# Kernel tuning notes

Hardware: AMD Instinct MI355X
Metric: run time of the kernel (lower is better)

The kernel has to match this reference:

```python
import jax, jax.numpy as jnp
import numpy as np

HIDDEN = 1280
NUM_HEADS = 16
NUM_KV_HEADS = 4
HEAD_DIM = 80
Q_SIZE = NUM_HEADS * HEAD_DIM          # 1280
KV_SIZE = NUM_KV_HEADS * HEAD_DIM      # 320
QKV_OUT = Q_SIZE + 2 * KV_SIZE         # 1920
R_SOFTPLUS_0 = 1.442695041


def setup_inputs() -> dict:
    key = jax.random.key(0)
    ks = jax.random.split(key, 6)
    B, S = 4, 2048
    return {
        "hidden_states": jax.random.normal(ks[0], (B, S, HIDDEN), dtype=jnp.float32),
        "scaling": jax.random.normal(ks[1], (HEAD_DIM,), dtype=jnp.float32),
        "qkv_w": jax.random.normal(ks[2], (QKV_OUT, HIDDEN), dtype=jnp.float32) * (1.0 / np.sqrt(HIDDEN)),
        "qkv_b": jax.random.normal(ks[3], (QKV_OUT,), dtype=jnp.float32) * 0.01,
        "o_w": jax.random.normal(ks[4], (HIDDEN, Q_SIZE), dtype=jnp.float32) * (1.0 / np.sqrt(Q_SIZE)),
        "o_b": jax.random.normal(ks[5], (HIDDEN,), dtype=jnp.float32) * 0.01,
    }


def reference(hidden_states, scaling, qkv_w, qkv_b, o_w, o_b):
    B, S, _ = hidden_states.shape
    qkv = hidden_states @ qkv_w.T + qkv_b                      # [B,S,1920]
    xq = qkv[..., :Q_SIZE].reshape(B, S, NUM_HEADS, HEAD_DIM)
    xk = qkv[..., Q_SIZE:Q_SIZE + KV_SIZE].reshape(B, S, NUM_KV_HEADS, HEAD_DIM)
    xv = qkv[..., Q_SIZE + KV_SIZE:].reshape(B, S, NUM_KV_HEADS, HEAD_DIM)
    # learned per-head-dim scaling: (r_softplus_0/sqrt(d)) * softplus(scaling)
    scale = (R_SOFTPLUS_0 / np.sqrt(HEAD_DIM)) * jax.nn.softplus(scaling)
    xq = xq * scale[None, None, None, :]
    # GQA: expand kv heads to match query heads (repeat_interleave on head dim)
    nq_per_kv = NUM_HEADS // NUM_KV_HEADS
    k = jnp.repeat(xk, nq_per_kv, axis=2)                      # [B,S,H,d]
    v = jnp.repeat(xv, nq_per_kv, axis=2)
    scores = jnp.einsum("bqhd,bkhd->bhqk", xq, k)              # [B,H,S,S]
    probs = jax.nn.softmax(scores.astype(jnp.float32), axis=-1).astype(xq.dtype)
    out = jnp.einsum("bhqk,bkhd->bqhd", probs, v)              # [B,S,H,d]
    out = out.reshape(B, S, Q_SIZE)
    return out @ o_w.T + o_b
```

## Files before the change

### kernel.cpp

```cpp
#include <hip/hip_runtime.h>

#define HIDDEN 1280
#define QOUT   1920
#define QSIZE  1280
#define KVSIZE 320
#define NHEAD  16
#define NKV    4
#define DH     80
#define SEQ    2048
#define BATCH  4
#define MTOT   (BATCH * SEQ)
#define NT64   (SEQ / 64)
#define KTILE_ELEMS 6144
#define VTILE_ELEMS 5120

typedef __attribute__((ext_vector_type(8))) short bf16x8;
typedef __attribute__((ext_vector_type(4))) short bf16x4;
typedef __attribute__((ext_vector_type(4))) float f32x4;

__device__ __forceinline__ unsigned short f2bf(float x) {
  union { float f; unsigned u; } v; v.f = x;
  unsigned r = v.u + 0x7fffu + ((v.u >> 16) & 1u);
  return (unsigned short)(r >> 16);
}

__device__ __forceinline__ unsigned packbf(float a, float b) {
  union { float f; unsigned u; } ua, ub;
  ua.f = a; ub.f = b;
  return __builtin_amdgcn_perm(ub.u + 0x8000u, ua.u + 0x8000u, 0x07060302u);
}

__device__ __forceinline__ unsigned packbf_t(float a, float b) {
  union { float f; unsigned u; } ua, ub;
  ua.f = a; ub.f = b;
  return __builtin_amdgcn_perm(ub.u, ua.u, 0x07060302u);
}

__device__ __forceinline__ float exp2x(float x) {
#if __has_builtin(__builtin_amdgcn_exp2f)
  return __builtin_amdgcn_exp2f(x);
#else
  return exp2f(x);
#endif
}

__device__ __forceinline__ void async_copy16(const void* g, void* lds) {
  __builtin_amdgcn_global_load_lds(
      (const __attribute__((address_space(1))) unsigned int*)g,
      (__attribute__((address_space(3))) unsigned int*)lds, 16, 0, 0);
}

#define HSB   (MTOT * HIDDEN / 4 / 256)
#define QWB   (QOUT * HIDDEN / 4 / 256)
#define OWB   (HIDDEN * QSIZE / 4 / 256)
__global__ __launch_bounds__(256) void prep_k(const float* __restrict__ hs,
                                              const float* __restrict__ qkv_w,
                                              const float* __restrict__ o_w,
                                              const float* __restrict__ scaling,
                                              unsigned short* __restrict__ hs_bf,
                                              unsigned short* __restrict__ qkvw_bf,
                                              unsigned short* __restrict__ ow_bf,
                                              float* __restrict__ cs) {
  const int bid = blockIdx.x, tid = threadIdx.x;
  const float* src; unsigned short* dst; int i;
  if (bid < HSB)            { src = hs;    dst = hs_bf;   i = bid * 256 + tid; }
  else if (bid < HSB + QWB) { src = qkv_w; dst = qkvw_bf; i = (bid - HSB) * 256 + tid; }
  else if (bid < HSB + QWB + OWB) { src = o_w; dst = ow_bf; i = (bid - HSB - QWB) * 256 + tid; }
  else {
    int n = (bid - HSB - QWB - OWB) * 256 + tid;
    if (n < QOUT) {
      float v = 1.0f;
      if (n < QSIZE) {
        float x = scaling[n % DH];
        float sp = (x > 20.f) ? x : log1pf(__expf(x));
        v = 1.442695041f * 1.442695041f * 0.11180339887f * sp;
      }
      cs[n] = v;
    }
    return;
  }
  float4 v = ((const float4*)src)[i];
  ushort4 o;
  o.x = f2bf(v.x); o.y = f2bf(v.y); o.z = f2bf(v.z); o.w = f2bf(v.w);
  ((ushort4*)dst)[i] = o;
}

template <bool OUT_BF16, bool USE_SCALE>
__global__ __launch_bounds__(512) void gemm_bt(const unsigned short* __restrict__ A,
                                               const unsigned short* __restrict__ Bt,
                                               const float* __restrict__ bias,
                                               const float* __restrict__ colscale,
                                               void* __restrict__ Cout,
                                               int M, int N, int K) {
  __shared__ unsigned short As[256 * 64];
  __shared__ unsigned short Bs[128 * 64];
  const int tid  = threadIdx.x;
  const int wave = tid >> 6, lane = tid & 63;
  const int r = lane & 15, quad = lane >> 4;
  const int xm = r & 7;
  const int m0 = blockIdx.y * 256, n0 = blockIdx.x * 128;
  const int rm = (wave >> 1) * 64, cn = (wave & 1) * 64;

  f32x4 acc[4][4];
#pragma unroll
  for (int i = 0; i < 4; ++i)
#pragma unroll
    for (int j = 0; j < 4; ++j) acc[i][j] = f32x4{0.f, 0.f, 0.f, 0.f};

  for (int k0 = 0; k0 < K; k0 += 64) {
    __syncthreads();
#pragma unroll
    for (int j = 0; j < 4; ++j) {
      const int c = tid + j * 512;
      const int row = c >> 3, sp = c & 7;
      const int sd = (sp ^ (row & 7)) * 8;
      async_copy16(A + (size_t)(m0 + row) * K + k0 + sd, &As[c * 8]);
    }
#pragma unroll
    for (int j = 0; j < 2; ++j) {
      const int c = tid + j * 512;
      const int row = c >> 3, sp = c & 7;
      const int sd = (sp ^ (row & 7)) * 8;
      async_copy16(Bt + (size_t)(n0 + row) * K + k0 + sd, &Bs[c * 8]);
    }
    __syncthreads();
#pragma unroll
    for (int kk = 0; kk < 2; ++kk) {
      bf16x8 af[4], bfr[4];
#pragma unroll
      for (int mi = 0; mi < 4; ++mi)
        af[mi] = *(const bf16x8*)&As[(rm + mi * 16 + r) * 64 + ((kk * 4 + quad) ^ xm) * 8];
#pragma unroll
      for (int ni = 0; ni < 4; ++ni)
        bfr[ni] = *(const bf16x8*)&Bs[(cn + ni * 16 + r) * 64 + ((kk * 4 + quad) ^ xm) * 8];
#pragma unroll
      for (int mi = 0; mi < 4; ++mi)
#pragma unroll
        for (int ni = 0; ni < 4; ++ni)
          acc[mi][ni] = __builtin_amdgcn_mfma_f32_16x16x32_bf16(af[mi], bfr[ni], acc[mi][ni], 0, 0, 0);
    }
  }

#pragma unroll
  for (int ni = 0; ni < 4; ++ni) {
    const int n = n0 + cn + ni * 16 + r;
    const float bn = bias[n];
    const float sc = USE_SCALE ? colscale[n] : 1.0f;
#pragma unroll
    for (int mi = 0; mi < 4; ++mi) {
#pragma unroll
      for (int reg = 0; reg < 4; ++reg) {
        const int m = m0 + rm + mi * 16 + quad * 4 + reg;
        const float v = (acc[mi][ni][reg] + bn) * sc;
        if (OUT_BF16)
          ((unsigned short*)Cout)[(size_t)m * N + n] = f2bf(v);
        else
          ((float*)Cout)[(size_t)m * N + n] = v;
      }
    }
  }
}

__global__ __launch_bounds__(256) void kvpack(const unsigned short* __restrict__ qkv,
                                              unsigned short* __restrict__ Kp,
                                              unsigned short* __restrict__ Vp) {
  const int st = blockIdx.x, kvh = blockIdx.y, b = blockIdx.z;
  const int tid = threadIdx.x;
  unsigned short* kout = Kp + (size_t)((b * NKV + kvh) * NT64 + st) * KTILE_ELEMS;
#pragma unroll
  for (int j = 0; j < 3; ++j) {
    int c = tid + j * 256;
    int row = c / 12, cir = c - row * 12;
    int kk = cir >> 2, sp = cir & 3;
    int sd = sp ^ ((row >> 1) & 3);
    int d0 = kk * 32 + sd * 8;
    int skey = (row >> 5) * 32 + ((row >> 2) & 3) * 8 + ((row >> 4) & 1) * 4 + (row & 3);
    uint4 v = {0, 0, 0, 0};
    if (d0 < DH)
      v = *(const uint4*)&qkv[(size_t)(b * SEQ + st * 64 + skey) * QOUT +
                              QSIZE + kvh * DH + d0];
    *(uint4*)&kout[row * 96 + kk * 32 + sp * 8] = v;
  }
  __shared__ unsigned short tile[64][88];
  for (int c = tid; c < 640; c += 256) {
    int row = c / 10, seg = c % 10;
    uint4 v = *(const uint4*)&qkv[(size_t)(b * SEQ + st * 64 + row) * QOUT +
                                  QSIZE + KVSIZE + kvh * DH + seg * 8];
    *(uint4*)&tile[row][seg * 8] = v;
  }
  __syncthreads();
  unsigned short* vout = Vp + (size_t)((b * NKV + kvh) * NT64 + st) * VTILE_ELEMS;
  for (int c = tid; c < 5120; c += 256) {
    int d = c >> 6, key = c & 63;
    vout[d * 64 + (key ^ ((d & 7) << 3))] = tile[key][d];
  }
}

__global__ __launch_bounds__(256, 2) void attn(const unsigned short* __restrict__ qkv,
                                               const unsigned short* __restrict__ Kp,
                                               const unsigned short* __restrict__ Vp,
                                               unsigned short* __restrict__ att) {
  const int qt = blockIdx.x, h = blockIdx.y, b = blockIdx.z;
  const int kvh = h >> 2;
  const int tid = threadIdx.x;
  const int wave = tid >> 6, lane = tid & 63;
  const int r = lane & 15, quad = lane >> 4;
  const int sq8 = (quad ^ ((r >> 1) & 3)) * 8;

  __shared__ unsigned short Ks[64 * 96];
  __shared__ unsigned short Vs[96 * 64];

  {
    const uint4 ones = {0x3F803F80u, 0x3F803F80u, 0x3F803F80u, 0x3F803F80u};
    for (int c = tid; c < 128; c += 256)
      *(uint4*)&Vs[80 * 64 + c * 8] = ones;
  }

  const int qbase = qt * 256 + wave * 64;
  bf16x8 qb[4][3];
#pragma unroll
  for (int t = 0; t < 4; ++t)
#pragma unroll
    for (int kk = 0; kk < 3; ++kk)
      qb[t][kk] = *(const bf16x8*)&qkv[(size_t)(b * SEQ + qbase + t * 16 + r) * QOUT +
                                       h * DH + kk * 32 + quad * 8];

  f32x4 o_acc[6][4];
#pragma unroll
  for (int i = 0; i < 6; ++i)
#pragma unroll
    for (int t = 0; t < 4; ++t) o_acc[i][t] = f32x4{0.f, 0.f, 0.f, 0.f};

  const unsigned short* kp = Kp + (size_t)((b * NKV + kvh) * NT64) * KTILE_ELEMS;
  const unsigned short* vp = Vp + (size_t)((b * NKV + kvh) * NT64) * VTILE_ELEMS;

  for (int kt = 0; kt < NT64; ++kt) {
    __syncthreads();
#pragma unroll
    for (int j = 0; j < 3; ++j)
      async_copy16(kp + (size_t)kt * KTILE_ELEMS + (tid + j * 256) * 8,
                   &Ks[(tid + j * 256) * 8]);
#pragma unroll
    for (int j = 0; j < 3; ++j) {
      int c = tid + j * 256;
      if (c < 640)
        async_copy16(vp + (size_t)kt * VTILE_ELEMS + c * 8, &Vs[c * 8]);
    }
    __syncthreads();

#pragma unroll
    for (int ntp = 0; ntp < 2; ++ntp) {
      uint4 pw[4];
      {
        bf16x8 ka[3];
#pragma unroll
        for (int kk = 0; kk < 3; ++kk)
          ka[kk] = *(const bf16x8*)&Ks[(ntp * 32 + r) * 96 + kk * 32 + sq8];
#pragma unroll
        for (int t = 0; t < 4; ++t) {
          f32x4 s = f32x4{0.f, 0.f, 0.f, 0.f};
#pragma unroll
          for (int kk = 0; kk < 3; ++kk)
            s = __builtin_amdgcn_mfma_f32_16x16x32_bf16(ka[kk], qb[t][kk], s, 0, 0, 0);
          pw[t].x = packbf_t(exp2x(s[0]), exp2x(s[1]));
          pw[t].y = packbf_t(exp2x(s[2]), exp2x(s[3]));
        }
      }
      {
        bf16x8 ka[3];
#pragma unroll
        for (int kk = 0; kk < 3; ++kk)
          ka[kk] = *(const bf16x8*)&Ks[(ntp * 32 + 16 + r) * 96 + kk * 32 + sq8];
#pragma unroll
        for (int t = 0; t < 4; ++t) {
          f32x4 s = f32x4{0.f, 0.f, 0.f, 0.f};
#pragma unroll
          for (int kk = 0; kk < 3; ++kk)
            s = __builtin_amdgcn_mfma_f32_16x16x32_bf16(ka[kk], qb[t][kk], s, 0, 0, 0);
          pw[t].z = packbf_t(exp2x(s[0]), exp2x(s[1]));
          pw[t].w = packbf_t(exp2x(s[2]), exp2x(s[3]));
        }
      }

#pragma unroll
      for (int nt2 = 0; nt2 < 6; ++nt2) {
        bf16x8 va = *(const bf16x8*)&Vs[(nt2 * 16 + r) * 64 +
                                        (((ntp * 4 + quad) ^ (r & 7)) << 3)];
#pragma unroll
        for (int t = 0; t < 4; ++t) {
          union { uint4 u; bf16x8 v; } pv; pv.u = pw[t];
          o_acc[nt2][t] = __builtin_amdgcn_mfma_f32_16x16x32_bf16(va, pv.v, o_acc[nt2][t], 0, 0, 0);
        }
      }
    }
  }

#pragma unroll
  for (int t = 0; t < 4; ++t) {
    const float il = 1.0f / o_acc[5][t][0];
    const size_t q = (size_t)(b * SEQ + qbase + t * 16 + r);
#pragma unroll
    for (int nt2 = 0; nt2 < 5; ++nt2) {
      uint2 w;
      w.x = packbf(o_acc[nt2][t][0] * il, o_acc[nt2][t][1] * il);
      w.y = packbf(o_acc[nt2][t][2] * il, o_acc[nt2][t][3] * il);
      *(uint2*)&att[q * QSIZE + h * DH + nt2 * 16 + quad * 4] = w;
    }
  }
}

extern "C" void kernel_launch(void* const* d_in, const int* in_sizes, int n_in,
                              void* d_out, int out_size, void* d_ws, size_t ws_size,
                              hipStream_t stream) {
  const float* hs      = (const float*)d_in[0];
  const float* scaling = (const float*)d_in[1];
  const float* qkv_w   = (const float*)d_in[2];
  const float* qkv_b   = (const float*)d_in[3];
  const float* o_w     = (const float*)d_in[4];
  const float* o_b     = (const float*)d_in[5];

  char* p = (char*)d_ws;
  unsigned short* hs_bf   = (unsigned short*)p; p += (size_t)MTOT * HIDDEN * 2;
  unsigned short* qkvw_bf = (unsigned short*)p; p += (size_t)QOUT * HIDDEN * 2;
  unsigned short* ow_bf   = (unsigned short*)p; p += (size_t)HIDDEN * QSIZE * 2;
  float* cscale           = (float*)p;          p += (size_t)QOUT * 4;
  unsigned short* qkv     = (unsigned short*)p; p += (size_t)MTOT * QOUT * 2;
  unsigned short* Kp      = (unsigned short*)p; p += (size_t)BATCH * NKV * NT64 * KTILE_ELEMS * 2;
  unsigned short* Vp      = (unsigned short*)p; p += (size_t)BATCH * NKV * NT64 * VTILE_ELEMS * 2;
  unsigned short* att     = hs_bf;

  prep_k<<<HSB + QWB + OWB + 8, 256, 0, stream>>>(hs, qkv_w, o_w, scaling,
                                                  hs_bf, qkvw_bf, ow_bf, cscale);

  dim3 g1(QOUT / 128, MTOT / 256);
  gemm_bt<true, true><<<g1, 512, 0, stream>>>(hs_bf, qkvw_bf, qkv_b, cscale, qkv,
                                              MTOT, QOUT, HIDDEN);
  dim3 gp(NT64, NKV, BATCH);
  kvpack<<<gp, 256, 0, stream>>>(qkv, Kp, Vp);
  dim3 g3(SEQ / 256, NHEAD, BATCH);
  attn<<<g3, 256, 0, stream>>>(qkv, Kp, Vp, att);
  dim3 g4(QSIZE / 128, MTOT / 256);
  gemm_bt<false, false><<<g4, 512, 0, stream>>>(att, ow_bf, o_b, nullptr, d_out,
                                                MTOT, QSIZE, HIDDEN);
}
```

Measured before the change: 283.6 us.

## Double-buffer K/V tiles in attention and split queries across eight waves

The attention kernel now keeps two LDS buffers for K and V and starts the async copy of the next key tile before computing on the current one. This overlaps global-to-LDS transfer with MFMA work and needs only one barrier per iteration. The block grows to 512 threads, each wave handling 32 queries instead of 64. That halves the per-wave accumulator and Q registers so more waves can hide latency, at the cost of less reuse of each K/V LDS fragment and twice the LDS footprint.

```diff
diff --git a/kernel.cpp b/kernel.cpp
--- a/kernel.cpp
+++ b/kernel.cpp
@@ -196,7 +196,7 @@
   }
 }
 
-__global__ __launch_bounds__(256, 2) void attn(const unsigned short* __restrict__ qkv,
+__global__ __launch_bounds__(512, 4) void attn(const unsigned short* __restrict__ qkv,
                                                const unsigned short* __restrict__ Kp,
                                                const unsigned short* __restrict__ Vp,
                                                unsigned short* __restrict__ att) {
@@ -207,57 +207,59 @@
   const int r = lane & 15, quad = lane >> 4;
   const int sq8 = (quad ^ ((r >> 1) & 3)) * 8;
 
-  __shared__ unsigned short Ks[64 * 96];
-  __shared__ unsigned short Vs[96 * 64];
+  __shared__ unsigned short Ks[2][64 * 96];
+  __shared__ unsigned short Vs[2][96 * 64];
 
   {
     const uint4 ones = {0x3F803F80u, 0x3F803F80u, 0x3F803F80u, 0x3F803F80u};
-    for (int c = tid; c < 128; c += 256)
-      *(uint4*)&Vs[80 * 64 + c * 8] = ones;
-  }
-
-  const int qbase = qt * 256 + wave * 64;
-  bf16x8 qb[4][3];
-#pragma unroll
-  for (int t = 0; t < 4; ++t)
+    for (int c = tid; c < 256; c += 512)
+      *(uint4*)&Vs[c >> 7][80 * 64 + (c & 127) * 8] = ones;
+  }
+
+  const int qbase = qt * 256 + wave * 32;
+  bf16x8 qb[2][3];
+#pragma unroll
+  for (int t = 0; t < 2; ++t)
 #pragma unroll
     for (int kk = 0; kk < 3; ++kk)
       qb[t][kk] = *(const bf16x8*)&qkv[(size_t)(b * SEQ + qbase + t * 16 + r) * QOUT +
                                        h * DH + kk * 32 + quad * 8];
 
-  f32x4 o_acc[6][4];
+  f32x4 o_acc[6][2];
 #pragma unroll
   for (int i = 0; i < 6; ++i)
 #pragma unroll
-    for (int t = 0; t < 4; ++t) o_acc[i][t] = f32x4{0.f, 0.f, 0.f, 0.f};
+    for (int t = 0; t < 2; ++t) o_acc[i][t] = f32x4{0.f, 0.f, 0.f, 0.f};
 
   const unsigned short* kp = Kp + (size_t)((b * NKV + kvh) * NT64) * KTILE_ELEMS;
   const unsigned short* vp = Vp + (size_t)((b * NKV + kvh) * NT64) * VTILE_ELEMS;
 
+#define STAGE(bufi, kt_) do {                                                   \
+    const unsigned short* kpt = kp + (size_t)(kt_) * KTILE_ELEMS;               \
+    async_copy16(kpt + tid * 8, &Ks[bufi][tid * 8]);                            \
+    if (tid < 256) async_copy16(kpt + (tid + 512) * 8, &Ks[bufi][(tid + 512) * 8]); \
+    const unsigned short* vpt = vp + (size_t)(kt_) * VTILE_ELEMS;               \
+    async_copy16(vpt + tid * 8, &Vs[bufi][tid * 8]);                            \
+    if (tid < 128) async_copy16(vpt + (tid + 512) * 8, &Vs[bufi][(tid + 512) * 8]); \
+  } while (0)
+
+  STAGE(0, 0);
+  __syncthreads();
+
   for (int kt = 0; kt < NT64; ++kt) {
-    __syncthreads();
-#pragma unroll
-    for (int j = 0; j < 3; ++j)
-      async_copy16(kp + (size_t)kt * KTILE_ELEMS + (tid + j * 256) * 8,
-                   &Ks[(tid + j * 256) * 8]);
-#pragma unroll
-    for (int j = 0; j < 3; ++j) {
-      int c = tid + j * 256;
-      if (c < 640)
-        async_copy16(vp + (size_t)kt * VTILE_ELEMS + c * 8, &Vs[c * 8]);
-    }
-    __syncthreads();
+    const int cur = kt & 1;
+    if (kt + 1 < NT64) STAGE(cur ^ 1, kt + 1);
 
 #pragma unroll
     for (int ntp = 0; ntp < 2; ++ntp) {
-      uint4 pw[4];
+      uint4 pw[2];
       {
         bf16x8 ka[3];
 #pragma unroll
         for (int kk = 0; kk < 3; ++kk)
-          ka[kk] = *(const bf16x8*)&Ks[(ntp * 32 + r) * 96 + kk * 32 + sq8];
-#pragma unroll
-        for (int t = 0; t < 4; ++t) {
+          ka[kk] = *(const bf16x8*)&Ks[cur][(ntp * 32 + r) * 96 + kk * 32 + sq8];
+#pragma unroll
+        for (int t = 0; t < 2; ++t) {
           f32x4 s = f32x4{0.f, 0.f, 0.f, 0.f};
 #pragma unroll
           for (int kk = 0; kk < 3; ++kk)
@@ -270,9 +272,9 @@
         bf16x8 ka[3];
 #pragma unroll
         for (int kk = 0; kk < 3; ++kk)
-          ka[kk] = *(const bf16x8*)&Ks[(ntp * 32 + 16 + r) * 96 + kk * 32 + sq8];
-#pragma unroll
-        for (int t = 0; t < 4; ++t) {
+          ka[kk] = *(const bf16x8*)&Ks[cur][(ntp * 32 + 16 + r) * 96 + kk * 32 + sq8];
+#pragma unroll
+        for (int t = 0; t < 2; ++t) {
           f32x4 s = f32x4{0.f, 0.f, 0.f, 0.f};
 #pragma unroll
           for (int kk = 0; kk < 3; ++kk)
@@ -284,19 +286,21 @@
 
 #pragma unroll
       for (int nt2 = 0; nt2 < 6; ++nt2) {
-        bf16x8 va = *(const bf16x8*)&Vs[(nt2 * 16 + r) * 64 +
-                                        (((ntp * 4 + quad) ^ (r & 7)) << 3)];
-#pragma unroll
-        for (int t = 0; t < 4; ++t) {
+        bf16x8 va = *(const bf16x8*)&Vs[cur][(nt2 * 16 + r) * 64 +
+                                             (((ntp * 4 + quad) ^ (r & 7)) << 3)];
+#pragma unroll
+        for (int t = 0; t < 2; ++t) {
           union { uint4 u; bf16x8 v; } pv; pv.u = pw[t];
           o_acc[nt2][t] = __builtin_amdgcn_mfma_f32_16x16x32_bf16(va, pv.v, o_acc[nt2][t], 0, 0, 0);
         }
       }
     }
-  }
-
-#pragma unroll
-  for (int t = 0; t < 4; ++t) {
+    __syncthreads();
+  }
+#undef STAGE
+
+#pragma unroll
+  for (int t = 0; t < 2; ++t) {
     const float il = 1.0f / o_acc[5][t][0];
     const size_t q = (size_t)(b * SEQ + qbase + t * 16 + r);
 #pragma unroll
@@ -338,7 +342,7 @@
   dim3 gp(NT64, NKV, BATCH);
   kvpack<<<gp, 256, 0, stream>>>(qkv, Kp, Vp);
   dim3 g3(SEQ / 256, NHEAD, BATCH);
-  attn<<<g3, 256, 0, stream>>>(qkv, Kp, Vp, att);
+  attn<<<g3, 512, 0, stream>>>(qkv, Kp, Vp, att);
   dim3 g4(QSIZE / 128, MTOT / 256);
   gemm_bt<false, false><<<g4, 512, 0, stream>>>(att, ow_bf, o_b, nullptr, d_out,
                                                 MTOT, QSIZE, HIDDEN);
```

Result: no change. 278.2 us (-1.9%).
